# Kernel tuning notes

Hardware: AMD Instinct MI355X
Metric: run time of the kernel (lower is better)

The kernel has to match this reference:

```python
import jax, jax.numpy as jnp
import numpy as np

N_NODES = 100000

def setup_inputs() -> dict:
    key = jax.random.key(0)
    k1, k2, k3, k4, k5 = jax.random.split(key, 5)
    node_emb = jax.random.normal(k1, (100000, 128), dtype=jnp.float32)
    edge_weight = jax.random.uniform(k2, (1600000,), dtype=jnp.float32)
    src = jax.random.randint(k3, (1600000,), 0, 100000, dtype=jnp.int32)
    dst = jax.random.randint(k4, (1600000,), 0, 100000, dtype=jnp.int32)
    W = jax.random.normal(k5, (128, 128), dtype=jnp.float32) * (1.0 / np.sqrt(128))
    return {"node_emb": node_emb, "edge_weight": edge_weight, "src": src, "dst": dst, "W": W}

def reference(node_emb, edge_weight, src, dst, W):
    # u_mul_e: gather source features, scale by per-edge scalar weight
    msg = node_emb[src] * edge_weight[:, None]          # [E, d]
    # sum reduce into destination nodes (scatter-add / segment-sum)
    agg = jax.ops.segment_sum(msg, dst, num_segments=N_NODES)  # [N, d]
    # linear_out (no bias): agg @ W^T (torch Linear applies x @ W.T)
    return agg @ W.T
```

## Files before the change

kernel.cpp:

```cpp
#include <hip/hip_runtime.h>
#include <cstdint>

typedef unsigned short u16;
typedef unsigned int   u32;

#define DIM     128
#define TPITCH  136
#define BSH     8
#define BSIZE   256
#define NBK_MAX 512
#define CHUNK   4096
#define FBS     128
#define CAP     2560

__device__ __forceinline__ u16 f2bf(float x) {
    u32 u = __float_as_uint(x);
    u32 r = u + 0x7FFFu + ((u >> 16) & 1u);
    return (u16)(r >> 16);
}

typedef __attribute__((ext_vector_type(8))) short bfrag;
typedef __attribute__((ext_vector_type(4))) float f32x4;
typedef __attribute__((ext_vector_type(2))) float f32x2;

__global__ __launch_bounds__(256) void k_count_transform(
    const float* __restrict__ A, const float* __restrict__ W,
    u16* __restrict__ Tb,
    const int* __restrict__ dst, int* __restrict__ cnt,
    int n, int E, int nCntBlk, int NBK)
{
    __shared__ u16 Wb[DIM * TPITCH];

    if (blockIdx.x < nCntBlk) {
        int* hist = (int*)Wb;
        for (int i = threadIdx.x; i < NBK; i += 256) hist[i] = 0;
        __syncthreads();
        const int base = blockIdx.x * CHUNK;
        const int end  = min(base + CHUNK, E);
        for (int i = base + threadIdx.x; i < end; i += 256)
            atomicAdd(&hist[dst[i] >> BSH], 1);
        __syncthreads();
        for (int b = threadIdx.x; b < NBK; b += 256)
            cnt[b * nCntBlk + blockIdx.x] = hist[b];
        return;
    }

    {
        const int j  = threadIdx.x >> 1;
        const int k0 = (threadIdx.x & 1) << 6;
        const float* wr = W + j * DIM + k0;
        u16* wo = Wb + j * TPITCH + k0;
#pragma unroll
        for (int k = 0; k < 64; k += 4) {
            float4 v = *(const float4*)(wr + k);
            ushort4 h;
            h.x = f2bf(v.x); h.y = f2bf(v.y); h.z = f2bf(v.z); h.w = f2bf(v.w);
            *(ushort4*)(wo + k) = h;
        }
    }
    __syncthreads();

    const int wave = threadIdx.x >> 6;
    const int lane = threadIdx.x & 63;
    const int quad = lane >> 4;
    const int l16  = lane & 15;

    const int r0b = (blockIdx.x - nCntBlk) << 6;
    const int r0  = r0b + (wave << 4);
    const bool active = (r0 < n);
    f32x4 acc[8];
#pragma unroll
    for (int c = 0; c < 8; ++c) acc[c] = (f32x4)(0.f);

    if (active) {
        const int ar = min(r0 + l16, n - 1);
        const float* arow = A + (size_t)ar * DIM;
#pragma unroll
        for (int s = 0; s < 4; ++s) {
            const int koff = (s << 5) + (quad << 3);
            const float4 f0 = *(const float4*)(arow + koff);
            const float4 f1 = *(const float4*)(arow + koff + 4);
            bfrag a;
            a[0] = (short)f2bf(f0.x); a[1] = (short)f2bf(f0.y);
            a[2] = (short)f2bf(f0.z); a[3] = (short)f2bf(f0.w);
            a[4] = (short)f2bf(f1.x); a[5] = (short)f2bf(f1.y);
            a[6] = (short)f2bf(f1.z); a[7] = (short)f2bf(f1.w);
#pragma unroll
            for (int c = 0; c < 8; ++c) {
                const int nn = (c << 4) + l16;
                const bfrag b = *(const bfrag*)(Wb + nn * TPITCH + koff);
                acc[c] = __builtin_amdgcn_mfma_f32_16x16x32_bf16(a, b, acc[c], 0, 0, 0);
            }
        }
    }

    __syncthreads();

    if (active) {
        const int rl0 = (wave << 4) + (quad << 2);
#pragma unroll
        for (int r = 0; r < 4; ++r) {
            u16* trow = Wb + (rl0 + r) * TPITCH + l16;
#pragma unroll
            for (int c = 0; c < 8; ++c)
                trow[c << 4] = f2bf(acc[c][r]);
        }
    }
    __syncthreads();

    {
        const int rl  = threadIdx.x >> 2;
        const int row = r0b + rl;
        if (row < n) {
            const float4* sp = (const float4*)(Wb + rl * TPITCH + ((threadIdx.x & 3) << 5));
            float4* dp = (float4*)(Tb + (size_t)row * DIM + ((threadIdx.x & 3) << 5));
            dp[0] = sp[0];
            dp[1] = sp[1];
            dp[2] = sp[2];
            dp[3] = sp[3];
        }
    }
}

__global__ __launch_bounds__(256) void k_rowsum(
    const int* __restrict__ cnt, int* __restrict__ tot, int nCntBlk)
{
    __shared__ int red[256];
    const int t = threadIdx.x;
    const int* row = cnt + blockIdx.x * nCntBlk;
    int s = 0;
    for (int i = t; i < nCntBlk; i += 256) s += row[i];
    red[t] = s; __syncthreads();
    for (int o = 128; o; o >>= 1) {
        if (t < o) red[t] += red[t + o];
        __syncthreads();
    }
    if (t == 0) tot[blockIdx.x] = red[0];
}

__global__ __launch_bounds__(512) void k_scan_all(
    const int* __restrict__ tot, int* __restrict__ bucketStart,
    int* __restrict__ cnt, int NBK, int nCntBlk, int E)
{
    __shared__ int sc[512];
    __shared__ int bs;
    const int t = threadIdx.x;
    const int b = blockIdx.x;

    const int v = (t < NBK) ? tot[t] : 0;
    sc[t] = v; __syncthreads();
    for (int d = 1; d < 512; d <<= 1) {
        int u = (t >= d) ? sc[t - d] : 0;
        __syncthreads();
        sc[t] += u;
        __syncthreads();
    }
    if (t == b) bs = sc[t] - v;
    if (b == 0) {
        if (t < NBK) bucketStart[t] = sc[t] - v;
        if (t == 0)  bucketStart[NBK] = E;
    }
    __syncthreads();

    int* row = cnt + b * nCntBlk;
    const int rv = (t < nCntBlk) ? row[t] : 0;
    sc[t] = rv; __syncthreads();
    for (int d = 1; d < 512; d <<= 1) {
        int u = (t >= d) ? sc[t - d] : 0;
        __syncthreads();
        sc[t] += u;
        __syncthreads();
    }
    if (t < nCntBlk) row[t] = bs + sc[t] - rv;
}

__global__ __launch_bounds__(512) void k_scatter(
    const int* __restrict__ src, const int* __restrict__ dst,
    const float* __restrict__ w, const int* __restrict__ cnt,
    const int* __restrict__ bucketStart,
    int2* __restrict__ es1, int E, int nCntBlk, int NBK)
{
    __shared__ int2 buf[CHUNK];
    __shared__ u16  bid[CHUNK];
    __shared__ int  gbase[NBK_MAX];
    __shared__ int  lbase[NBK_MAX];
    __shared__ int  lpos[NBK_MAX];
    __shared__ int  sc[512];

    const int blk  = blockIdx.x;
    const int base = blk * CHUNK;
    const int end  = min(base + CHUNK, E);
    const int len  = end - base;
    const int t    = threadIdx.x;

    int mylen = 0;
    if (t < NBK) {
        const int g = cnt[t * nCntBlk + blk];
        gbase[t] = g;
        const int nxt = (blk + 1 < nCntBlk) ? cnt[t * nCntBlk + blk + 1]
                                            : bucketStart[t + 1];
        mylen = nxt - g;
    }
    sc[t] = (t < NBK) ? mylen : 0;
    __syncthreads();
    for (int d = 1; d < 512; d <<= 1) {
        int v = (t >= d) ? sc[t - d] : 0;
        __syncthreads();
        sc[t] += v;
        __syncthreads();
    }
    if (t < NBK) {
        const int ex = sc[t] - mylen;
        lbase[t] = ex;
        lpos[t]  = ex;
    }
    __syncthreads();

    for (int i = base + t; i < end; i += 512) {
        const int d   = dst[i];
        const int bkt = d >> BSH;
        const int p   = atomicAdd(&lpos[bkt], 1);
        buf[p] = make_int2(src[i] | ((d & (BSIZE - 1)) << 20),
                           __float_as_int(w[i]));
        bid[p] = (u16)bkt;
    }
    __syncthreads();

    for (int i = t; i < len; i += 512) {
        const int bkt = bid[i];
        es1[gbase[bkt] + (i - lbase[bkt])] = buf[i];
    }
}

__global__ __launch_bounds__(512) void gnn_aggregate(
    const u16* __restrict__ Tb, const int* __restrict__ bucketStart,
    const int2* __restrict__ es1, float* __restrict__ out, int n)
{
    __shared__ int2 buf[CAP];
    __shared__ int  cnt[FBS];
    __shared__ int  loff[FBS + 1];
    __shared__ int  cur[FBS];
    __shared__ int  sc[FBS];

    const int f    = blockIdx.x;
    const int c    = f >> 1;
    const int hbit = (f & 1) << 7;
    const int s    = bucketStart[c], e = bucketStart[c + 1];
    const int v0   = f << 7;
    const int t    = threadIdx.x;
    const int lane = t & 63;
    const int wv   = t >> 6;
    const u32* Tw  = (const u32*)Tb;

    if (t < FBS) cnt[t] = 0;
    __syncthreads();
    for (int i = s + t; i < e; i += 512) {
        const int d8 = (es1[i].x >> 20) & 255;
        if ((d8 & 128) == hbit) atomicAdd(&cnt[d8 & 127], 1);
    }
    __syncthreads();

    int myc = 0;
    if (t < FBS) { myc = cnt[t]; sc[t] = myc; }
    __syncthreads();
    for (int d = 1; d < FBS; d <<= 1) {
        int u = 0;
        if (t < FBS && t >= d) u = sc[t - d];
        __syncthreads();
        if (t < FBS) sc[t] += u;
        __syncthreads();
    }
    if (t < FBS) {
        const int ex = sc[t] - myc;
        loff[t] = ex; cur[t] = ex;
        if (t == FBS - 1) loff[FBS] = sc[t];
    }
    __syncthreads();
    const int kept = loff[FBS];

    if (kept <= CAP) {
        for (int i = s + t; i < e; i += 512) {
            const int2 ev = es1[i];
            const int d8 = (ev.x >> 20) & 255;
            if ((d8 & 128) == hbit) {
                const int p = atomicAdd(&cur[d8 & 127], 1);
                buf[p] = make_int2(ev.x & 0xFFFFF, ev.y);
            }
        }
        __syncthreads();

        for (int nt = 0; nt < 16; ++nt) {
            const int tn = (wv << 4) + nt;
            const int v  = v0 + tn;
            if (v >= n) break;
            const int kb = loff[tn], ke = loff[tn + 1];
            float ax0 = 0.f, ay0 = 0.f, ax1 = 0.f, ay1 = 0.f;

            int i = kb;
            for (; i + 7 < ke; i += 8) {
                const int2 e0 = buf[i],     e1 = buf[i + 1], e2 = buf[i + 2], e3 = buf[i + 3];
                const int2 e4 = buf[i + 4], e5 = buf[i + 5], e6 = buf[i + 6], e7 = buf[i + 7];
                const u32 t0 = Tw[(size_t)e0.x * 64 + lane];
                const u32 t1 = Tw[(size_t)e1.x * 64 + lane];
                const u32 t2 = Tw[(size_t)e2.x * 64 + lane];
                const u32 t3 = Tw[(size_t)e3.x * 64 + lane];
                const u32 t4 = Tw[(size_t)e4.x * 64 + lane];
                const u32 t5 = Tw[(size_t)e5.x * 64 + lane];
                const u32 t6 = Tw[(size_t)e6.x * 64 + lane];
                const u32 t7 = Tw[(size_t)e7.x * 64 + lane];
                const float w0 = __int_as_float(e0.y), w1 = __int_as_float(e1.y);
                const float w2 = __int_as_float(e2.y), w3 = __int_as_float(e3.y);
                const float w4 = __int_as_float(e4.y), w5 = __int_as_float(e5.y);
                const float w6 = __int_as_float(e6.y), w7 = __int_as_float(e7.y);
                ax0 += w0 * __uint_as_float(t0 << 16);
                ay0 += w0 * __uint_as_float(t0 & 0xFFFF0000u);
                ax1 += w1 * __uint_as_float(t1 << 16);
                ay1 += w1 * __uint_as_float(t1 & 0xFFFF0000u);
                ax0 += w2 * __uint_as_float(t2 << 16);
                ay0 += w2 * __uint_as_float(t2 & 0xFFFF0000u);
                ax1 += w3 * __uint_as_float(t3 << 16);
                ay1 += w3 * __uint_as_float(t3 & 0xFFFF0000u);
                ax0 += w4 * __uint_as_float(t4 << 16);
                ay0 += w4 * __uint_as_float(t4 & 0xFFFF0000u);
                ax1 += w5 * __uint_as_float(t5 << 16);
                ay1 += w5 * __uint_as_float(t5 & 0xFFFF0000u);
                ax0 += w6 * __uint_as_float(t6 << 16);
                ay0 += w6 * __uint_as_float(t6 & 0xFFFF0000u);
                ax1 += w7 * __uint_as_float(t7 << 16);
                ay1 += w7 * __uint_as_float(t7 & 0xFFFF0000u);
            }
            for (; i + 3 < ke; i += 4) {
                const int2 e0 = buf[i], e1 = buf[i + 1], e2 = buf[i + 2], e3 = buf[i + 3];
                const u32 t0 = Tw[(size_t)e0.x * 64 + lane];
                const u32 t1 = Tw[(size_t)e1.x * 64 + lane];
                const u32 t2 = Tw[(size_t)e2.x * 64 + lane];
                const u32 t3 = Tw[(size_t)e3.x * 64 + lane];
                const float w0 = __int_as_float(e0.y), w1 = __int_as_float(e1.y);
                const float w2 = __int_as_float(e2.y), w3 = __int_as_float(e3.y);
                ax0 += w0 * __uint_as_float(t0 << 16);
                ay0 += w0 * __uint_as_float(t0 & 0xFFFF0000u);
                ax1 += w1 * __uint_as_float(t1 << 16);
                ay1 += w1 * __uint_as_float(t1 & 0xFFFF0000u);
                ax0 += w2 * __uint_as_float(t2 << 16);
                ay0 += w2 * __uint_as_float(t2 & 0xFFFF0000u);
                ax1 += w3 * __uint_as_float(t3 << 16);
                ay1 += w3 * __uint_as_float(t3 & 0xFFFF0000u);
            }
            for (; i < ke; ++i) {
                const int2 ev = buf[i];
                const u32 tv = Tw[(size_t)ev.x * 64 + lane];
                const float w0 = __int_as_float(ev.y);
                ax0 += w0 * __uint_as_float(tv << 16);
                ay0 += w0 * __uint_as_float(tv & 0xFFFF0000u);
            }

            f32x2 r;
            r[0] = ax0 + ax1;
            r[1] = ay0 + ay1;
            __builtin_nontemporal_store(r, (f32x2*)(out + (size_t)v * DIM + 2 * lane));
        }
    } else {
        for (int nt = 0; nt < 16; ++nt) {
            const int tn = (wv << 4) + nt;
            const int v  = v0 + tn;
            if (v >= n) break;
            const int want = hbit | tn;
            float ax = 0.f, ay = 0.f;
            for (int i = s; i < e; ++i) {
                const int2 ev = es1[i];
                if (((ev.x >> 20) & 255) == want) {
                    const u32 tv = Tw[(size_t)(ev.x & 0xFFFFF) * 64 + lane];
                    const float wgt = __int_as_float(ev.y);
                    ax += wgt * __uint_as_float(tv << 16);
                    ay += wgt * __uint_as_float(tv & 0xFFFF0000u);
                }
            }
            f32x2 r; r[0] = ax; r[1] = ay;
            __builtin_nontemporal_store(r, (f32x2*)(out + (size_t)v * DIM + 2 * lane));
        }
    }
}

extern "C" void kernel_launch(void* const* d_in, const int* in_sizes, int n_in,
                              void* d_out, int out_size, void* d_ws, size_t ws_size,
                              hipStream_t stream)
{
    const float* node_emb = (const float*)d_in[0];
    const float* ew       = (const float*)d_in[1];
    const int*   src      = (const int*)d_in[2];
    const int*   dst      = (const int*)d_in[3];
    const float* W        = (const float*)d_in[4];
    float* out = (float*)d_out;

    const int n = in_sizes[0] / DIM;
    const int E = in_sizes[1];
    const int NBK = (n + BSIZE - 1) >> BSH;
    const int nCntBlk = (E + CHUNK - 1) / CHUNK;
    const int M = NBK * nCntBlk;
    const int nfine = (n + FBS - 1) / FBS;

    char* ws = (char*)d_ws;
    size_t o = 0;
    u16* Tb = (u16*)(ws + o);  o += (((size_t)n * DIM * sizeof(u16)) + 255) & ~255ULL;
    int* cnt = (int*)(ws + o); o += (((size_t)M * sizeof(int)) + 255) & ~255ULL;
    int* tot = (int*)(ws + o); o += (((size_t)NBK * sizeof(int)) + 255) & ~255ULL;
    int* bucketStart = (int*)(ws + o); o += (((size_t)(NBK + 1) * sizeof(int)) + 255) & ~255ULL;
    int2* es1 = (int2*)(ws + o);

    const int ntiles = (n + 63) >> 6;

    k_count_transform<<<nCntBlk + ntiles, 256, 0, stream>>>(
        node_emb, W, Tb, dst, cnt, n, E, nCntBlk, NBK);

    k_rowsum<<<NBK, 256, 0, stream>>>(cnt, tot, nCntBlk);
    k_scan_all<<<NBK, 512, 0, stream>>>(tot, bucketStart, cnt, NBK, nCntBlk, E);

    k_scatter<<<nCntBlk, 512, 0, stream>>>(src, dst, ew, cnt, bucketStart,
                                           es1, E, nCntBlk, NBK);

    gnn_aggregate<<<nfine, 512, 0, stream>>>(Tb, bucketStart, es1, out, n);
}
```

Measured before the change: 227.8 us.

## Replace per-block count matrix and two-level scan with atomic bucket cursors

The count kernel now adds its per-block bucket histograms straight into global bucket totals with atomics. The rowsum kernel and the multi-block scan over the count matrix are replaced by a single-block scan that writes bucket starts and cursors. Each scatter block recomputes its own local histogram and reserves its slice in each bucket with an atomicAdd on the cursor. This removes one launch and the traffic on the large count matrix, but dst is read a second time and edge order within a bucket becomes nondeterministic, so float summation order may change between runs.

```diff
diff --git a/kernel.cpp b/kernel.cpp
--- a/kernel.cpp
+++ b/kernel.cpp
@@ -26,7 +26,7 @@
 __global__ __launch_bounds__(256) void k_count_transform(
     const float* __restrict__ A, const float* __restrict__ W,
     u16* __restrict__ Tb,
-    const int* __restrict__ dst, int* __restrict__ cnt,
+    const int* __restrict__ dst, int* __restrict__ tot,
     int n, int E, int nCntBlk, int NBK)
 {
     __shared__ u16 Wb[DIM * TPITCH];
@@ -40,8 +40,10 @@
         for (int i = base + threadIdx.x; i < end; i += 256)
             atomicAdd(&hist[dst[i] >> BSH], 1);
         __syncthreads();
-        for (int b = threadIdx.x; b < NBK; b += 256)
-            cnt[b * nCntBlk + blockIdx.x] = hist[b];
+        for (int b = threadIdx.x; b < NBK; b += 256) {
+            const int h = hist[b];
+            if (h) atomicAdd(&tot[b], h);
+        }
         return;
     }
 
@@ -68,6 +70,7 @@
     const int r0b = (blockIdx.x - nCntBlk) << 6;
     const int r0  = r0b + (wave << 4);
     const bool active = (r0 < n);
+
     f32x4 acc[8];
 #pragma unroll
     for (int c = 0; c < 8; ++c) acc[c] = (f32x4)(0.f);
@@ -122,31 +125,12 @@
     }
 }
 
-__global__ __launch_bounds__(256) void k_rowsum(
-    const int* __restrict__ cnt, int* __restrict__ tot, int nCntBlk)
-{
-    __shared__ int red[256];
+__global__ __launch_bounds__(512) void k_scan(
+    const int* __restrict__ tot, int* __restrict__ bucketStart,
+    int* __restrict__ cursor, int NBK, int E)
+{
+    __shared__ int sc[512];
     const int t = threadIdx.x;
-    const int* row = cnt + blockIdx.x * nCntBlk;
-    int s = 0;
-    for (int i = t; i < nCntBlk; i += 256) s += row[i];
-    red[t] = s; __syncthreads();
-    for (int o = 128; o; o >>= 1) {
-        if (t < o) red[t] += red[t + o];
-        __syncthreads();
-    }
-    if (t == 0) tot[blockIdx.x] = red[0];
-}
-
-__global__ __launch_bounds__(512) void k_scan_all(
-    const int* __restrict__ tot, int* __restrict__ bucketStart,
-    int* __restrict__ cnt, int NBK, int nCntBlk, int E)
-{
-    __shared__ int sc[512];
-    __shared__ int bs;
-    const int t = threadIdx.x;
-    const int b = blockIdx.x;
-
     const int v = (t < NBK) ? tot[t] : 0;
     sc[t] = v; __syncthreads();
     for (int d = 1; d < 512; d <<= 1) {
@@ -155,33 +139,22 @@
         sc[t] += u;
         __syncthreads();
     }
-    if (t == b) bs = sc[t] - v;
-    if (b == 0) {
-        if (t < NBK) bucketStart[t] = sc[t] - v;
-        if (t == 0)  bucketStart[NBK] = E;
-    }
-    __syncthreads();
-
-    int* row = cnt + b * nCntBlk;
-    const int rv = (t < nCntBlk) ? row[t] : 0;
-    sc[t] = rv; __syncthreads();
-    for (int d = 1; d < 512; d <<= 1) {
-        int u = (t >= d) ? sc[t - d] : 0;
-        __syncthreads();
-        sc[t] += u;
-        __syncthreads();
-    }
-    if (t < nCntBlk) row[t] = bs + sc[t] - rv;
+    if (t < NBK) {
+        const int excl = sc[t] - v;
+        bucketStart[t] = excl;
+        cursor[t] = excl;
+    }
+    if (t == 0) bucketStart[NBK] = E;
 }
 
 __global__ __launch_bounds__(512) void k_scatter(
     const int* __restrict__ src, const int* __restrict__ dst,
-    const float* __restrict__ w, const int* __restrict__ cnt,
-    const int* __restrict__ bucketStart,
-    int2* __restrict__ es1, int E, int nCntBlk, int NBK)
+    const float* __restrict__ w, int* __restrict__ cursor,
+    int2* __restrict__ es1, int E, int NBK)
 {
     __shared__ int2 buf[CHUNK];
     __shared__ u16  bid[CHUNK];
+    __shared__ int  hist[NBK_MAX];
     __shared__ int  gbase[NBK_MAX];
     __shared__ int  lbase[NBK_MAX];
     __shared__ int  lpos[NBK_MAX];
@@ -193,26 +166,26 @@
     const int len  = end - base;
     const int t    = threadIdx.x;
 
-    int mylen = 0;
+    if (t < NBK) hist[t] = 0;
+    __syncthreads();
+    for (int i = base + t; i < end; i += 512)
+        atomicAdd(&hist[dst[i] >> BSH], 1);
+    __syncthreads();
+
+    const int v = (t < NBK) ? hist[t] : 0;
+    sc[t] = v;
+    __syncthreads();
+    for (int d = 1; d < 512; d <<= 1) {
+        int u = (t >= d) ? sc[t - d] : 0;
+        __syncthreads();
+        sc[t] += u;
+        __syncthreads();
+    }
     if (t < NBK) {
-        const int g = cnt[t * nCntBlk + blk];
-        gbase[t] = g;
-        const int nxt = (blk + 1 < nCntBlk) ? cnt[t * nCntBlk + blk + 1]
-                                            : bucketStart[t + 1];
-        mylen = nxt - g;
-    }
-    sc[t] = (t < NBK) ? mylen : 0;
-    __syncthreads();
-    for (int d = 1; d < 512; d <<= 1) {
-        int v = (t >= d) ? sc[t - d] : 0;
-        __syncthreads();
-        sc[t] += v;
-        __syncthreads();
-    }
-    if (t < NBK) {
-        const int ex = sc[t] - mylen;
+        const int ex = sc[t] - v;
         lbase[t] = ex;
         lpos[t]  = ex;
+        if (v) gbase[t] = atomicAdd(&cursor[t], v);
     }
     __syncthreads();
 
@@ -396,27 +369,26 @@
     const int E = in_sizes[1];
     const int NBK = (n + BSIZE - 1) >> BSH;
     const int nCntBlk = (E + CHUNK - 1) / CHUNK;
-    const int M = NBK * nCntBlk;
     const int nfine = (n + FBS - 1) / FBS;
 
     char* ws = (char*)d_ws;
     size_t o = 0;
     u16* Tb = (u16*)(ws + o);  o += (((size_t)n * DIM * sizeof(u16)) + 255) & ~255ULL;
-    int* cnt = (int*)(ws + o); o += (((size_t)M * sizeof(int)) + 255) & ~255ULL;
     int* tot = (int*)(ws + o); o += (((size_t)NBK * sizeof(int)) + 255) & ~255ULL;
     int* bucketStart = (int*)(ws + o); o += (((size_t)(NBK + 1) * sizeof(int)) + 255) & ~255ULL;
+    int* cursor = (int*)(ws + o); o += (((size_t)NBK * sizeof(int)) + 255) & ~255ULL;
     int2* es1 = (int2*)(ws + o);
 
     const int ntiles = (n + 63) >> 6;
 
+    hipMemsetAsync(tot, 0, (size_t)NBK * sizeof(int), stream);
+
     k_count_transform<<<nCntBlk + ntiles, 256, 0, stream>>>(
-        node_emb, W, Tb, dst, cnt, n, E, nCntBlk, NBK);
-
-    k_rowsum<<<NBK, 256, 0, stream>>>(cnt, tot, nCntBlk);
-    k_scan_all<<<NBK, 512, 0, stream>>>(tot, bucketStart, cnt, NBK, nCntBlk, E);
-
-    k_scatter<<<nCntBlk, 512, 0, stream>>>(src, dst, ew, cnt, bucketStart,
-                                           es1, E, nCntBlk, NBK);
+        node_emb, W, Tb, dst, tot, n, E, nCntBlk, NBK);
+
+    k_scan<<<1, 512, 0, stream>>>(tot, bucketStart, cursor, NBK, E);
+
+    k_scatter<<<nCntBlk, 512, 0, stream>>>(src, dst, ew, cursor, es1, E, NBK);
 
     gnn_aggregate<<<nfine, 512, 0, stream>>>(Tb, bucketStart, es1, out, n);
 }
```

Result: slower. 235.1 us (+3.2%).

## Shrink dst buckets to 128 nodes so aggregate blocks read only their edges

Applied to the files above, without the earlier changes.

Halves the destination bucket size so each aggregation block owns exactly one bucket. Previously two blocks each scanned a shared 256-node bucket and discarded the half that was not theirs, so every edge record was read twice. The scan and scatter kernels now loop over more than 512 buckets with a carried prefix to handle the larger bucket count. The cost is a longer scan in every scatter block and fewer edges per bucket per chunk, which makes the es1 writes less coalesced.

```diff
diff --git a/kernel.cpp b/kernel.cpp
--- a/kernel.cpp
+++ b/kernel.cpp
@@ -6,9 +6,9 @@
 
 #define DIM     128
 #define TPITCH  136
-#define BSH     8
-#define BSIZE   256
-#define NBK_MAX 512
+#define BSH     7
+#define BSIZE   128
+#define NBK_MAX 800
 #define CHUNK   4096
 #define FBS     128
 #define CAP     2560
@@ -68,6 +68,7 @@
     const int r0b = (blockIdx.x - nCntBlk) << 6;
     const int r0  = r0b + (wave << 4);
     const bool active = (r0 < n);
+
     f32x4 acc[8];
 #pragma unroll
     for (int c = 0; c < 8; ++c) acc[c] = (f32x4)(0.f);
@@ -144,23 +145,30 @@
 {
     __shared__ int sc[512];
     __shared__ int bs;
+    __shared__ int carry;
     const int t = threadIdx.x;
     const int b = blockIdx.x;
-
-    const int v = (t < NBK) ? tot[t] : 0;
-    sc[t] = v; __syncthreads();
-    for (int d = 1; d < 512; d <<= 1) {
-        int u = (t >= d) ? sc[t - d] : 0;
-        __syncthreads();
-        sc[t] += u;
-        __syncthreads();
-    }
-    if (t == b) bs = sc[t] - v;
-    if (b == 0) {
-        if (t < NBK) bucketStart[t] = sc[t] - v;
-        if (t == 0)  bucketStart[NBK] = E;
-    }
-    __syncthreads();
+    if (t == 0) carry = 0;
+    __syncthreads();
+
+    for (int c0 = 0; c0 < NBK; c0 += 512) {
+        const int idx = c0 + t;
+        const int v = (idx < NBK) ? tot[idx] : 0;
+        sc[t] = v; __syncthreads();
+        for (int d = 1; d < 512; d <<= 1) {
+            int u = (t >= d) ? sc[t - d] : 0;
+            __syncthreads();
+            sc[t] += u;
+            __syncthreads();
+        }
+        const int excl = carry + sc[t] - v;
+        if (idx == b) bs = excl;
+        if (b == 0 && idx < NBK) bucketStart[idx] = excl;
+        __syncthreads();
+        if (t == 0) carry += sc[511];
+        __syncthreads();
+    }
+    if (b == 0 && t == 0) bucketStart[NBK] = E;
 
     int* row = cnt + b * nCntBlk;
     const int rv = (t < nCntBlk) ? row[t] : 0;
@@ -186,6 +194,7 @@
     __shared__ int  lbase[NBK_MAX];
     __shared__ int  lpos[NBK_MAX];
     __shared__ int  sc[512];
+    __shared__ int  carry;
 
     const int blk  = blockIdx.x;
     const int base = blk * CHUNK;
@@ -193,28 +202,36 @@
     const int len  = end - base;
     const int t    = threadIdx.x;
 
-    int mylen = 0;
-    if (t < NBK) {
-        const int g = cnt[t * nCntBlk + blk];
-        gbase[t] = g;
-        const int nxt = (blk + 1 < nCntBlk) ? cnt[t * nCntBlk + blk + 1]
-                                            : bucketStart[t + 1];
-        mylen = nxt - g;
-    }
-    sc[t] = (t < NBK) ? mylen : 0;
-    __syncthreads();
-    for (int d = 1; d < 512; d <<= 1) {
-        int v = (t >= d) ? sc[t - d] : 0;
-        __syncthreads();
-        sc[t] += v;
-        __syncthreads();
-    }
-    if (t < NBK) {
-        const int ex = sc[t] - mylen;
-        lbase[t] = ex;
-        lpos[t]  = ex;
-    }
-    __syncthreads();
+    if (t == 0) carry = 0;
+    __syncthreads();
+
+    for (int c0 = 0; c0 < NBK; c0 += 512) {
+        const int idx = c0 + t;
+        int v = 0;
+        if (idx < NBK) {
+            const int g = cnt[idx * nCntBlk + blk];
+            gbase[idx] = g;
+            const int nxt = (blk + 1 < nCntBlk) ? cnt[idx * nCntBlk + blk + 1]
+                                                : bucketStart[idx + 1];
+            v = nxt - g;
+        }
+        sc[t] = v;
+        __syncthreads();
+        for (int d = 1; d < 512; d <<= 1) {
+            int u = (t >= d) ? sc[t - d] : 0;
+            __syncthreads();
+            sc[t] += u;
+            __syncthreads();
+        }
+        const int ex = carry + sc[t] - v;
+        if (idx < NBK) {
+            lbase[idx] = ex;
+            lpos[idx]  = ex;
+        }
+        __syncthreads();
+        if (t == 0) carry += sc[511];
+        __syncthreads();
+    }
 
     for (int i = base + t; i < end; i += 512) {
         const int d   = dst[i];
@@ -243,10 +260,9 @@
     __shared__ int  sc[FBS];
 
     const int f    = blockIdx.x;
-    const int c    = f >> 1;
-    const int hbit = (f & 1) << 7;
-    const int s    = bucketStart[c], e = bucketStart[c + 1];
-    const int v0   = f << 7;
+    const int s    = bucketStart[f], e = bucketStart[f + 1];
+    const int len  = e - s;
+    const int v0   = f << BSH;
     const int t    = threadIdx.x;
     const int lane = t & 63;
     const int wv   = t >> 6;
@@ -254,10 +270,8 @@
 
     if (t < FBS) cnt[t] = 0;
     __syncthreads();
-    for (int i = s + t; i < e; i += 512) {
-        const int d8 = (es1[i].x >> 20) & 255;
-        if ((d8 & 128) == hbit) atomicAdd(&cnt[d8 & 127], 1);
-    }
+    for (int i = s + t; i < e; i += 512)
+        atomicAdd(&cnt[(es1[i].x >> 20) & 127], 1);
     __syncthreads();
 
     int myc = 0;
@@ -276,16 +290,12 @@
         if (t == FBS - 1) loff[FBS] = sc[t];
     }
     __syncthreads();
-    const int kept = loff[FBS];
-
-    if (kept <= CAP) {
+
+    if (len <= CAP) {
         for (int i = s + t; i < e; i += 512) {
             const int2 ev = es1[i];
-            const int d8 = (ev.x >> 20) & 255;
-            if ((d8 & 128) == hbit) {
-                const int p = atomicAdd(&cur[d8 & 127], 1);
-                buf[p] = make_int2(ev.x & 0xFFFFF, ev.y);
-            }
+            const int p = atomicAdd(&cur[(ev.x >> 20) & 127], 1);
+            buf[p] = make_int2(ev.x & 0xFFFFF, ev.y);
         }
         __syncthreads();
 
@@ -364,11 +374,10 @@
             const int tn = (wv << 4) + nt;
             const int v  = v0 + tn;
             if (v >= n) break;
-            const int want = hbit | tn;
             float ax = 0.f, ay = 0.f;
             for (int i = s; i < e; ++i) {
                 const int2 ev = es1[i];
-                if (((ev.x >> 20) & 255) == want) {
+                if (((ev.x >> 20) & 127) == tn) {
                     const u32 tv = Tw[(size_t)(ev.x & 0xFFFFF) * 64 + lane];
                     const float wgt = __int_as_float(ev.y);
                     ax += wgt * __uint_as_float(tv << 16);
@@ -397,7 +406,6 @@
     const int NBK = (n + BSIZE - 1) >> BSH;
     const int nCntBlk = (E + CHUNK - 1) / CHUNK;
     const int M = NBK * nCntBlk;
-    const int nfine = (n + FBS - 1) / FBS;
 
     char* ws = (char*)d_ws;
     size_t o = 0;
@@ -418,5 +426,5 @@
     k_scatter<<<nCntBlk, 512, 0, stream>>>(src, dst, ew, cnt, bucketStart,
                                            es1, E, nCntBlk, NBK);
 
-    gnn_aggregate<<<nfine, 512, 0, stream>>>(Tb, bucketStart, es1, out, n);
-}
+    gnn_aggregate<<<NBK, 512, 0, stream>>>(Tb, bucketStart, es1, out, n);
+}
```

New measurement: 231.8 us. About the same (+1.8%).

## Fuse node feature transform into the scatter kernel instead of the count kernel

Applied to the files above, without the earlier changes.

The bf16 dense transform of node embeddings (node_emb @ W^T) now runs as extra blocks of the edge scatter kernel instead of the histogram count kernel, which becomes a standalone light kernel. Transform tiles grow to 128 rows per 512-thread block so they match the scatter kernel's block size, and both paths share one 48KB shared buffer. The aim is to overlap the independent GEMM with the heavier scatter phase rather than with the cheap count phase. In exchange, the larger shared-memory footprint and bigger blocks may lower occupancy for the transform blocks.

```diff
diff --git a/kernel.cpp b/kernel.cpp
--- a/kernel.cpp
+++ b/kernel.cpp
@@ -23,35 +23,148 @@
 typedef __attribute__((ext_vector_type(4))) float f32x4;
 typedef __attribute__((ext_vector_type(2))) float f32x2;
 
-__global__ __launch_bounds__(256) void k_count_transform(
+__global__ __launch_bounds__(256) void k_count(
+    const int* __restrict__ dst, int* __restrict__ cnt,
+    int E, int nCntBlk, int NBK)
+{
+    __shared__ int hist[NBK_MAX];
+    for (int i = threadIdx.x; i < NBK; i += 256) hist[i] = 0;
+    __syncthreads();
+    const int base = blockIdx.x * CHUNK;
+    const int end  = min(base + CHUNK, E);
+    for (int i = base + threadIdx.x; i < end; i += 256)
+        atomicAdd(&hist[dst[i] >> BSH], 1);
+    __syncthreads();
+    for (int b = threadIdx.x; b < NBK; b += 256)
+        cnt[b * nCntBlk + blockIdx.x] = hist[b];
+}
+
+__global__ __launch_bounds__(256) void k_rowsum(
+    const int* __restrict__ cnt, int* __restrict__ tot, int nCntBlk)
+{
+    __shared__ int red[256];
+    const int t = threadIdx.x;
+    const int* row = cnt + blockIdx.x * nCntBlk;
+    int s = 0;
+    for (int i = t; i < nCntBlk; i += 256) s += row[i];
+    red[t] = s; __syncthreads();
+    for (int o = 128; o; o >>= 1) {
+        if (t < o) red[t] += red[t + o];
+        __syncthreads();
+    }
+    if (t == 0) tot[blockIdx.x] = red[0];
+}
+
+__global__ __launch_bounds__(512) void k_scan_all(
+    const int* __restrict__ tot, int* __restrict__ bucketStart,
+    int* __restrict__ cnt, int NBK, int nCntBlk, int E)
+{
+    __shared__ int sc[512];
+    __shared__ int bs;
+    const int t = threadIdx.x;
+    const int b = blockIdx.x;
+
+    const int v = (t < NBK) ? tot[t] : 0;
+    sc[t] = v; __syncthreads();
+    for (int d = 1; d < 512; d <<= 1) {
+        int u = (t >= d) ? sc[t - d] : 0;
+        __syncthreads();
+        sc[t] += u;
+        __syncthreads();
+    }
+    if (t == b) bs = sc[t] - v;
+    if (b == 0) {
+        if (t < NBK) bucketStart[t] = sc[t] - v;
+        if (t == 0)  bucketStart[NBK] = E;
+    }
+    __syncthreads();
+
+    int* row = cnt + b * nCntBlk;
+    const int rv = (t < nCntBlk) ? row[t] : 0;
+    sc[t] = rv; __syncthreads();
+    for (int d = 1; d < 512; d <<= 1) {
+        int u = (t >= d) ? sc[t - d] : 0;
+        __syncthreads();
+        sc[t] += u;
+        __syncthreads();
+    }
+    if (t < nCntBlk) row[t] = bs + sc[t] - rv;
+}
+
+__global__ __launch_bounds__(512) void k_scatter_transform(
+    const int* __restrict__ src, const int* __restrict__ dst,
+    const float* __restrict__ w, const int* __restrict__ cnt,
+    const int* __restrict__ bucketStart, int2* __restrict__ es1,
     const float* __restrict__ A, const float* __restrict__ W,
     u16* __restrict__ Tb,
-    const int* __restrict__ dst, int* __restrict__ cnt,
     int n, int E, int nCntBlk, int NBK)
 {
-    __shared__ u16 Wb[DIM * TPITCH];
+    __shared__ __align__(16) char smem[49152];
+
+    const int t = threadIdx.x;
 
     if (blockIdx.x < nCntBlk) {
-        int* hist = (int*)Wb;
-        for (int i = threadIdx.x; i < NBK; i += 256) hist[i] = 0;
-        __syncthreads();
-        const int base = blockIdx.x * CHUNK;
+        int2* buf   = (int2*)smem;
+        u16*  bid   = (u16*)(smem + 32768);
+        int*  gbase = (int*)(smem + 40960);
+        int*  lbase = (int*)(smem + 43008);
+        int*  lpos  = (int*)(smem + 45056);
+        int*  sc    = (int*)(smem + 47104);
+
+        const int blk  = blockIdx.x;
+        const int base = blk * CHUNK;
         const int end  = min(base + CHUNK, E);
-        for (int i = base + threadIdx.x; i < end; i += 256)
-            atomicAdd(&hist[dst[i] >> BSH], 1);
-        __syncthreads();
-        for (int b = threadIdx.x; b < NBK; b += 256)
-            cnt[b * nCntBlk + blockIdx.x] = hist[b];
+        const int len  = end - base;
+
+        int mylen = 0;
+        if (t < NBK) {
+            const int g = cnt[t * nCntBlk + blk];
+            gbase[t] = g;
+            const int nxt = (blk + 1 < nCntBlk) ? cnt[t * nCntBlk + blk + 1]
+                                                : bucketStart[t + 1];
+            mylen = nxt - g;
+        }
+        sc[t] = (t < NBK) ? mylen : 0;
+        __syncthreads();
+        for (int d = 1; d < 512; d <<= 1) {
+            int v = (t >= d) ? sc[t - d] : 0;
+            __syncthreads();
+            sc[t] += v;
+            __syncthreads();
+        }
+        if (t < NBK) {
+            const int ex = sc[t] - mylen;
+            lbase[t] = ex;
+            lpos[t]  = ex;
+        }
+        __syncthreads();
+
+        for (int i = base + t; i < end; i += 512) {
+            const int d   = dst[i];
+            const int bkt = d >> BSH;
+            const int p   = atomicAdd(&lpos[bkt], 1);
+            buf[p] = make_int2(src[i] | ((d & (BSIZE - 1)) << 20),
+                               __float_as_int(w[i]));
+            bid[p] = (u16)bkt;
+        }
+        __syncthreads();
+
+        for (int i = t; i < len; i += 512) {
+            const int bkt = bid[i];
+            es1[gbase[bkt] + (i - lbase[bkt])] = buf[i];
+        }
         return;
     }
 
+    u16* Wb = (u16*)smem;
+
     {
-        const int j  = threadIdx.x >> 1;
-        const int k0 = (threadIdx.x & 1) << 6;
+        const int j  = t >> 2;
+        const int k0 = (t & 3) << 5;
         const float* wr = W + j * DIM + k0;
         u16* wo = Wb + j * TPITCH + k0;
 #pragma unroll
-        for (int k = 0; k < 64; k += 4) {
+        for (int k = 0; k < 32; k += 4) {
             float4 v = *(const float4*)(wr + k);
             ushort4 h;
             h.x = f2bf(v.x); h.y = f2bf(v.y); h.z = f2bf(v.z); h.w = f2bf(v.w);
@@ -60,14 +173,15 @@
     }
     __syncthreads();
 
-    const int wave = threadIdx.x >> 6;
-    const int lane = threadIdx.x & 63;
+    const int wave = t >> 6;
+    const int lane = t & 63;
     const int quad = lane >> 4;
     const int l16  = lane & 15;
 
-    const int r0b = (blockIdx.x - nCntBlk) << 6;
+    const int r0b = (blockIdx.x - nCntBlk) << 7;
     const int r0  = r0b + (wave << 4);
     const bool active = (r0 < n);
+
     f32x4 acc[8];
 #pragma unroll
     for (int c = 0; c < 8; ++c) acc[c] = (f32x4)(0.f);
@@ -109,126 +223,16 @@
     __syncthreads();
 
     {
-        const int rl  = threadIdx.x >> 2;
+        const int rl  = t >> 2;
         const int row = r0b + rl;
         if (row < n) {
-            const float4* sp = (const float4*)(Wb + rl * TPITCH + ((threadIdx.x & 3) << 5));
-            float4* dp = (float4*)(Tb + (size_t)row * DIM + ((threadIdx.x & 3) << 5));
+            const float4* sp = (const float4*)(Wb + rl * TPITCH + ((t & 3) << 5));
+            float4* dp = (float4*)(Tb + (size_t)row * DIM + ((t & 3) << 5));
             dp[0] = sp[0];
             dp[1] = sp[1];
             dp[2] = sp[2];
             dp[3] = sp[3];
         }
-    }
-}
-
-__global__ __launch_bounds__(256) void k_rowsum(
-    const int* __restrict__ cnt, int* __restrict__ tot, int nCntBlk)
-{
-    __shared__ int red[256];
-    const int t = threadIdx.x;
-    const int* row = cnt + blockIdx.x * nCntBlk;
-    int s = 0;
-    for (int i = t; i < nCntBlk; i += 256) s += row[i];
-    red[t] = s; __syncthreads();
-    for (int o = 128; o; o >>= 1) {
-        if (t < o) red[t] += red[t + o];
-        __syncthreads();
-    }
-    if (t == 0) tot[blockIdx.x] = red[0];
-}
-
-__global__ __launch_bounds__(512) void k_scan_all(
-    const int* __restrict__ tot, int* __restrict__ bucketStart,
-    int* __restrict__ cnt, int NBK, int nCntBlk, int E)
-{
-    __shared__ int sc[512];
-    __shared__ int bs;
-    const int t = threadIdx.x;
-    const int b = blockIdx.x;
-
-    const int v = (t < NBK) ? tot[t] : 0;
-    sc[t] = v; __syncthreads();
-    for (int d = 1; d < 512; d <<= 1) {
-        int u = (t >= d) ? sc[t - d] : 0;
-        __syncthreads();
-        sc[t] += u;
-        __syncthreads();
-    }
-    if (t == b) bs = sc[t] - v;
-    if (b == 0) {
-        if (t < NBK) bucketStart[t] = sc[t] - v;
-        if (t == 0)  bucketStart[NBK] = E;
-    }
-    __syncthreads();
-
-    int* row = cnt + b * nCntBlk;
-    const int rv = (t < nCntBlk) ? row[t] : 0;
-    sc[t] = rv; __syncthreads();
-    for (int d = 1; d < 512; d <<= 1) {
-        int u = (t >= d) ? sc[t - d] : 0;
-        __syncthreads();
-        sc[t] += u;
-        __syncthreads();
-    }
-    if (t < nCntBlk) row[t] = bs + sc[t] - rv;
-}
-
-__global__ __launch_bounds__(512) void k_scatter(
-    const int* __restrict__ src, const int* __restrict__ dst,
-    const float* __restrict__ w, const int* __restrict__ cnt,
-    const int* __restrict__ bucketStart,
-    int2* __restrict__ es1, int E, int nCntBlk, int NBK)
-{
-    __shared__ int2 buf[CHUNK];
-    __shared__ u16  bid[CHUNK];
-    __shared__ int  gbase[NBK_MAX];
-    __shared__ int  lbase[NBK_MAX];
-    __shared__ int  lpos[NBK_MAX];
-    __shared__ int  sc[512];
-
-    const int blk  = blockIdx.x;
-    const int base = blk * CHUNK;
-    const int end  = min(base + CHUNK, E);
-    const int len  = end - base;
-    const int t    = threadIdx.x;
-
-    int mylen = 0;
-    if (t < NBK) {
-        const int g = cnt[t * nCntBlk + blk];
-        gbase[t] = g;
-        const int nxt = (blk + 1 < nCntBlk) ? cnt[t * nCntBlk + blk + 1]
-                                            : bucketStart[t + 1];
-        mylen = nxt - g;
-    }
-    sc[t] = (t < NBK) ? mylen : 0;
-    __syncthreads();
-    for (int d = 1; d < 512; d <<= 1) {
-        int v = (t >= d) ? sc[t - d] : 0;
-        __syncthreads();
-        sc[t] += v;
-        __syncthreads();
-    }
-    if (t < NBK) {
-        const int ex = sc[t] - mylen;
-        lbase[t] = ex;
-        lpos[t]  = ex;
-    }
-    __syncthreads();
-
-    for (int i = base + t; i < end; i += 512) {
-        const int d   = dst[i];
-        const int bkt = d >> BSH;
-        const int p   = atomicAdd(&lpos[bkt], 1);
-        buf[p] = make_int2(src[i] | ((d & (BSIZE - 1)) << 20),
-                           __float_as_int(w[i]));
-        bid[p] = (u16)bkt;
-    }
-    __syncthreads();
-
-    for (int i = t; i < len; i += 512) {
-        const int bkt = bid[i];
-        es1[gbase[bkt] + (i - lbase[bkt])] = buf[i];
     }
 }
 
@@ -407,16 +411,16 @@
     int* bucketStart = (int*)(ws + o); o += (((size_t)(NBK + 1) * sizeof(int)) + 255) & ~255ULL;
     int2* es1 = (int2*)(ws + o);
 
-    const int ntiles = (n + 63) >> 6;
-
-    k_count_transform<<<nCntBlk + ntiles, 256, 0, stream>>>(
-        node_emb, W, Tb, dst, cnt, n, E, nCntBlk, NBK);
+    const int ntiles = (n + 127) >> 7;
+
+    k_count<<<nCntBlk, 256, 0, stream>>>(dst, cnt, E, nCntBlk, NBK);
 
     k_rowsum<<<NBK, 256, 0, stream>>>(cnt, tot, nCntBlk);
     k_scan_all<<<NBK, 512, 0, stream>>>(tot, bucketStart, cnt, NBK, nCntBlk, E);
 
-    k_scatter<<<nCntBlk, 512, 0, stream>>>(src, dst, ew, cnt, bucketStart,
-                                           es1, E, nCntBlk, NBK);
+    k_scatter_transform<<<nCntBlk + ntiles, 512, 0, stream>>>(
+        src, dst, ew, cnt, bucketStart, es1, node_emb, W, Tb,
+        n, E, nCntBlk, NBK);
 
     gnn_aggregate<<<nfine, 512, 0, stream>>>(Tb, bucketStart, es1, out, n);
 }
```

Result: faster. 214.5 us (-5.8%).
